# Kernel optimization log

Hardware: AMD Instinct MI355X
Metric: run time of the kernel (lower is better)

Reference implementation:

```python
import jax, jax.numpy as jnp
import numpy as np
from jax.ops import segment_sum, segment_max

# Graph layout: B contiguous graphs of NPER nodes each
N, B, NPER, E, K = 32768, 32, 1024, 524288, 32
IN_DIM, HID = 64, 64
H1, H2 = 4, 2
NEG_ATTN, NEG_ACT = 0.2, 0.01  # DGL GATConv leaky slope; module's LeakyReLU slope


def _gat(x, src, dst, W, al, ar, H, D):
    # DGL GATConv, no bias, no residual, dropout=0
    f = (x @ W).reshape(N, H, D)                      # [N,H,D]
    el = jnp.einsum('nhd,hd->nh', f, al)              # src attention term
    er = jnp.einsum('nhd,hd->nh', f, ar)              # dst attention term
    e = jax.nn.leaky_relu(el[src] + er[dst], NEG_ATTN)  # [E,H]
    m = segment_max(e, dst, num_segments=N)
    m = jnp.where(jnp.isfinite(m), m, 0.0)            # guard isolated nodes
    p = jnp.exp(e - m[dst])
    z = segment_sum(p, dst, num_segments=N)
    a = p / jnp.maximum(z[dst], 1e-9)                 # edge softmax over in-edges
    return segment_sum(a[:, :, None] * f[src], dst, num_segments=N)  # [N,H,D]


def _graphnorm(x, alpha, gamma, beta, eps=1e-5):
    # GraphNorm (Cai et al.): per-graph node normalization with learnable mean scale
    xb = x.reshape(B, NPER, *x.shape[1:])
    mean = xb.mean(axis=1, keepdims=True)
    c = xb - alpha * mean
    var = (c * c).mean(axis=1, keepdims=True)
    return (gamma * c / jnp.sqrt(var + eps) + beta).reshape(x.shape)


def _sortpool(x):
    # DGL SortPooling: sort each node's features ascending, pick top-K nodes by last channel
    xs = jnp.sort(x, axis=-1).reshape(B, NPER, -1)
    _, idx = jax.lax.top_k(xs[:, :, -1], K)           # [B,K]
    sel = jnp.take_along_axis(xs, idx[:, :, None], axis=1)  # [B,K,D]
    return sel.reshape(B, -1)


def setup_inputs() -> dict:
    key = jax.random.key(0)
    ks = jax.random.split(key, 16)
    rng = np.random.default_rng(0)
    # edges constrained within each contiguous graph block
    g = rng.integers(0, B, size=E)
    src = (g * NPER + rng.integers(0, NPER, size=E)).astype(np.int32)
    dst = (g * NPER + rng.integers(0, NPER, size=E)).astype(np.int32)
    s = 0.05
    return {
        'features': jax.random.normal(ks[0], (N, IN_DIM), jnp.float32),
        'src': jnp.asarray(src), 'dst': jnp.asarray(dst),
        'W1': jax.random.normal(ks[1], (IN_DIM, H1 * HID), jnp.float32) * s,
        'al1': jax.random.normal(ks[2], (H1, HID), jnp.float32) * s,
        'ar1': jax.random.normal(ks[3], (H1, HID), jnp.float32) * s,
        'W2': jax.random.normal(ks[4], (H1 * HID, H2 * HID), jnp.float32) * s,
        'al2': jax.random.normal(ks[5], (H2, HID), jnp.float32) * s,
        'ar2': jax.random.normal(ks[6], (H2, HID), jnp.float32) * s,
        'gn1_alpha': jnp.ones((HID,), jnp.float32),
        'gn1_gamma': jnp.ones((HID,), jnp.float32),
        'gn1_beta': jnp.zeros((HID,), jnp.float32),
        'gn2_alpha': jnp.ones((HID,), jnp.float32),
        'gn2_gamma': jnp.ones((HID,), jnp.float32),
        'gn2_beta': jnp.zeros((HID,), jnp.float32),
        'fc1_w': jax.random.normal(ks[7], (2 * K * HID, K * HID), jnp.float32) * 0.02,
        'fc1_b': jnp.zeros((K * HID,), jnp.float32),
        'fc2_w': jax.random.normal(ks[8], (K * HID, 16), jnp.float32) * 0.02,
        'fc2_b': jnp.zeros((16,), jnp.float32),
    }


def reference(features, src, dst, W1, al1, ar1, W2, al2, ar2,
              gn1_alpha, gn1_gamma, gn1_beta, gn2_alpha, gn2_gamma, gn2_beta,
              fc1_w, fc1_b, fc2_w, fc2_b):
    h1 = _gat(features, src, dst, W1, al1, ar1, H1, HID)          # [N,4,HID]
    h1 = jax.nn.leaky_relu(_graphnorm(h1, gn1_alpha, gn1_gamma, gn1_beta), NEG_ACT)
    r1 = _sortpool(h1.mean(1))                                    # [B,K*HID]
    h2 = _gat(h1.reshape(N, -1), src, dst, W2, al2, ar2, H2, HID)  # [N,2,HID]
    h2 = jax.nn.leaky_relu(_graphnorm(h2, gn2_alpha, gn2_gamma, gn2_beta), NEG_ACT)
    r = jnp.concatenate([r1, _sortpool(h2.mean(1))], axis=1)      # [B,2*K*HID]
    hidden = jax.nn.relu(r @ fc1_w + fc1_b)
    return hidden @ fc2_w + fc2_b                                 # [B,16]
```

## Files before the change

kernel.cpp:

```cpp
#include <hip/hip_runtime.h>
#include <math.h>

#define NNODES 32768
#define NGRAPH 32
#define NPERG  1024
#define KSEL   32
#define FC1_KS 64

__device__ inline float wave_reduce_sum(float v) {
  #pragma unroll
  for (int off = 32; off > 0; off >>= 1) v += __shfl_xor(v, off, 64);
  return v;
}
__device__ inline float wave_reduce_max(float v) {
  #pragma unroll
  for (int off = 32; off > 0; off >>= 1) v = fmaxf(v, __shfl_xor(v, off, 64));
  return v;
}

__global__ void csr_count(const int* __restrict__ dst, int* __restrict__ counts, int E_) {
  int e = blockIdx.x * 256 + threadIdx.x;
  if (e < E_) atomicAdd(&counts[dst[e]], 1);
}

__global__ void csr_scan(const int* __restrict__ counts, int* __restrict__ rowptr,
                         int* __restrict__ cursor) {
  __shared__ int partial[256];
  int tid = threadIdx.x;
  int base = tid * 128;
  int s = 0;
  for (int i = 0; i < 128; ++i) s += counts[base + i];
  partial[tid] = s;
  __syncthreads();
  for (int off = 1; off < 256; off <<= 1) {
    int t = (tid >= off) ? partial[tid - off] : 0;
    __syncthreads();
    partial[tid] += t;
    __syncthreads();
  }
  int run = partial[tid] - s;
  for (int i = 0; i < 128; ++i) {
    int c = counts[base + i];
    rowptr[base + i] = run;
    cursor[base + i] = run;
    run += c;
  }
  if (tid == 255) rowptr[NNODES] = run;
}

__global__ void csr_fill(const int* __restrict__ src, const int* __restrict__ dst,
                         int* __restrict__ cursor, int* __restrict__ csrsrc, int E_) {
  int e = blockIdx.x * 256 + threadIdx.x;
  if (e < E_) {
    int p = atomicAdd(&cursor[dst[e]], 1);
    csrsrc[p] = src[e];
  }
}

template <int K, int C, int H>
__global__ __launch_bounds__(256) void gemm_fused(
    const float* __restrict__ X, const float* __restrict__ W,
    const float* __restrict__ al, const float* __restrict__ ar,
    float* __restrict__ F, float* __restrict__ el, float* __restrict__ er) {
  __shared__ float Xs[16][68];
  __shared__ float Ws[16][64];
  __shared__ float redl[64][16];
  __shared__ float redr[64][16];
  const int tid = threadIdx.x;
  const int tx = tid & 15, ty = tid >> 4;
  const int bx = blockIdx.x;
  const int xcd = bx & 7, pos = bx >> 3;
  const int gph = xcd + (pos >> 4) * 8;
  const int row0 = (gph * 16 + (pos & 15)) * 64;
  const int col0 = blockIdx.y * 64;

  float acc[4][4];
  #pragma unroll
  for (int i = 0; i < 4; ++i)
    #pragma unroll
    for (int j = 0; j < 4; ++j) acc[i][j] = 0.f;

  const int rld = tid >> 2;
  const int kq = (tid & 3) * 4;
  const int kw = tid >> 4;
  const int cw = (tid & 15) * 4;

  for (int kt = 0; kt < K; kt += 16) {
    float4 xv = *(const float4*)&X[(size_t)(row0 + rld) * K + kt + kq];
    Xs[kq + 0][rld] = xv.x; Xs[kq + 1][rld] = xv.y;
    Xs[kq + 2][rld] = xv.z; Xs[kq + 3][rld] = xv.w;
    *(float4*)&Ws[kw][cw] = *(const float4*)&W[(size_t)(kt + kw) * C + col0 + cw];
    __syncthreads();
    #pragma unroll
    for (int k = 0; k < 16; ++k) {
      float xr[4], wr[4];
      #pragma unroll
      for (int i = 0; i < 4; ++i) xr[i] = Xs[k][ty * 4 + i];
      #pragma unroll
      for (int j = 0; j < 4; ++j) wr[j] = Ws[k][tx * 4 + j];
      #pragma unroll
      for (int i = 0; i < 4; ++i)
        #pragma unroll
        for (int j = 0; j < 4; ++j) acc[i][j] = fmaf(xr[i], wr[j], acc[i][j]);
    }
    __syncthreads();
  }

  float av[4], rv[4];
  #pragma unroll
  for (int j = 0; j < 4; ++j) { av[j] = al[col0 + tx * 4 + j]; rv[j] = ar[col0 + tx * 4 + j]; }
  #pragma unroll
  for (int i = 0; i < 4; ++i) {
    float4 o = make_float4(acc[i][0], acc[i][1], acc[i][2], acc[i][3]);
    *(float4*)&F[(size_t)(row0 + ty * 4 + i) * C + col0 + tx * 4] = o;
    float pl = acc[i][0] * av[0] + acc[i][1] * av[1] + acc[i][2] * av[2] + acc[i][3] * av[3];
    float pr = acc[i][0] * rv[0] + acc[i][1] * rv[1] + acc[i][2] * rv[2] + acc[i][3] * rv[3];
    redl[ty * 4 + i][tx] = pl;
    redr[ty * 4 + i][tx] = pr;
  }
  __syncthreads();
  if (tid < 64) {
    float s = 0.f, t = 0.f;
    #pragma unroll
    for (int x = 0; x < 16; ++x) { s += redl[tid][x]; t += redr[tid][x]; }
    el[(row0 + tid) * H + blockIdx.y] = s;
    er[(row0 + tid) * H + blockIdx.y] = t;
  }
}

template <int H>
__device__ inline void load_ev(const float* __restrict__ el, int s, float* ev) {
  if constexpr (H == 4) {
    float4 t = *(const float4*)(el + (size_t)s * 4);
    ev[0] = t.x; ev[1] = t.y; ev[2] = t.z; ev[3] = t.w;
  } else {
    float2 t = *(const float2*)(el + (size_t)s * 2);
    ev[0] = t.x; ev[1] = t.y;
  }
}

template <int H>
__global__ __launch_bounds__(256) void gat_agg(
    const float* __restrict__ F, const float* __restrict__ el,
    const float* __restrict__ er, const int* __restrict__ rowptr,
    const int* __restrict__ csrsrc, float* __restrict__ out) {
  __shared__ float plds[4][64][H];
  __shared__ int slds[4][64];
  const int wave = threadIdx.x >> 6;
  const int lane = threadIdx.x & 63;
  const int wg = blockIdx.x;
  const int xcd = wg & 7, pos = wg >> 3;
  const int g = xcd + (pos >> 8) * 8;
  const int n = g * NPERG + (pos & 255) * 4 + wave;
  const int beg = rowptr[n], end = rowptr[n + 1];
  const int hsel = (H == 4) ? (lane >> 4) : (lane >> 5);

  float erh[H];
  #pragma unroll
  for (int h = 0; h < H; ++h) erh[h] = er[n * H + h];

  float e0[H], mx[H];
  #pragma unroll
  for (int h = 0; h < H; ++h) e0[h] = -INFINITY;
  const int i0 = beg + lane;
  int s0 = 0;
  if (i0 < end) {
    s0 = csrsrc[i0];
    float ev[H];
    load_ev<H>(el, s0, ev);
    #pragma unroll
    for (int h = 0; h < H; ++h) {
      float e = ev[h] + erh[h];
      e0[h] = e >= 0.f ? e : 0.2f * e;
    }
  }
  #pragma unroll
  for (int h = 0; h < H; ++h) mx[h] = e0[h];
  for (int i = i0 + 64; i < end; i += 64) {
    int s = csrsrc[i];
    float ev[H];
    load_ev<H>(el, s, ev);
    #pragma unroll
    for (int h = 0; h < H; ++h) {
      float e = ev[h] + erh[h];
      e = e >= 0.f ? e : 0.2f * e;
      mx[h] = fmaxf(mx[h], e);
    }
  }
  #pragma unroll
  for (int h = 0; h < H; ++h) mx[h] = wave_reduce_max(mx[h]);

  float accv[H];
  float psum[H];
  #pragma unroll
  for (int h = 0; h < H; ++h) { accv[h] = 0.f; psum[h] = 0.f; }

  for (int cbeg = beg; cbeg < end; cbeg += 64) {
    int cnt = end - cbeg;
    if (cnt > 64) cnt = 64;
    float pv[H];
    int s = 0;
    #pragma unroll
    for (int h = 0; h < H; ++h) pv[h] = 0.f;
    if (lane < cnt) {
      if (cbeg == beg) {
        s = s0;
        #pragma unroll
        for (int h = 0; h < H; ++h) pv[h] = __expf(e0[h] - mx[h]);
      } else {
        s = csrsrc[cbeg + lane];
        float ev[H];
        load_ev<H>(el, s, ev);
        #pragma unroll
        for (int h = 0; h < H; ++h) {
          float e = ev[h] + erh[h];
          e = e >= 0.f ? e : 0.2f * e;
          pv[h] = __expf(e - mx[h]);
        }
      }
    }
    #pragma unroll
    for (int h = 0; h < H; ++h) psum[h] += wave_reduce_sum(pv[h]);
    slds[wave][lane] = s;
    if constexpr (H == 4)
      *(float4*)&plds[wave][lane][0] = make_float4(pv[0], pv[1], pv[2], pv[3]);
    else
      *(float2*)&plds[wave][lane][0] = make_float2(pv[0], pv[1]);
    __builtin_amdgcn_s_waitcnt(0);

    int j = 0;
    for (; j + 4 <= cnt; j += 4) {
      int ss0 = slds[wave][j + 0], ss1 = slds[wave][j + 1];
      int ss2 = slds[wave][j + 2], ss3 = slds[wave][j + 3];
      float pb0 = plds[wave][j + 0][hsel], pb1 = plds[wave][j + 1][hsel];
      float pb2 = plds[wave][j + 2][hsel], pb3 = plds[wave][j + 3][hsel];
      if constexpr (H == 4) {
        float4 f0 = *(const float4*)&F[(size_t)ss0 * 256 + lane * 4];
        float4 f1 = *(const float4*)&F[(size_t)ss1 * 256 + lane * 4];
        float4 f2 = *(const float4*)&F[(size_t)ss2 * 256 + lane * 4];
        float4 f3 = *(const float4*)&F[(size_t)ss3 * 256 + lane * 4];
        accv[0] = fmaf(pb0, f0.x, accv[0]); accv[1] = fmaf(pb0, f0.y, accv[1]);
        accv[2] = fmaf(pb0, f0.z, accv[2]); accv[3] = fmaf(pb0, f0.w, accv[3]);
        accv[0] = fmaf(pb1, f1.x, accv[0]); accv[1] = fmaf(pb1, f1.y, accv[1]);
        accv[2] = fmaf(pb1, f1.z, accv[2]); accv[3] = fmaf(pb1, f1.w, accv[3]);
        accv[0] = fmaf(pb2, f2.x, accv[0]); accv[1] = fmaf(pb2, f2.y, accv[1]);
        accv[2] = fmaf(pb2, f2.z, accv[2]); accv[3] = fmaf(pb2, f2.w, accv[3]);
        accv[0] = fmaf(pb3, f3.x, accv[0]); accv[1] = fmaf(pb3, f3.y, accv[1]);
        accv[2] = fmaf(pb3, f3.z, accv[2]); accv[3] = fmaf(pb3, f3.w, accv[3]);
      } else {
        float2 f0 = *(const float2*)&F[(size_t)ss0 * 128 + lane * 2];
        float2 f1 = *(const float2*)&F[(size_t)ss1 * 128 + lane * 2];
        float2 f2 = *(const float2*)&F[(size_t)ss2 * 128 + lane * 2];
        float2 f3 = *(const float2*)&F[(size_t)ss3 * 128 + lane * 2];
        accv[0] = fmaf(pb0, f0.x, accv[0]); accv[1] = fmaf(pb0, f0.y, accv[1]);
        accv[0] = fmaf(pb1, f1.x, accv[0]); accv[1] = fmaf(pb1, f1.y, accv[1]);
        accv[0] = fmaf(pb2, f2.x, accv[0]); accv[1] = fmaf(pb2, f2.y, accv[1]);
        accv[0] = fmaf(pb3, f3.x, accv[0]); accv[1] = fmaf(pb3, f3.y, accv[1]);
      }
    }
    for (; j < cnt; ++j) {
      int ss = slds[wave][j];
      float pb = plds[wave][j][hsel];
      if constexpr (H == 4) {
        float4 fv = *(const float4*)&F[(size_t)ss * 256 + lane * 4];
        accv[0] = fmaf(pb, fv.x, accv[0]); accv[1] = fmaf(pb, fv.y, accv[1]);
        accv[2] = fmaf(pb, fv.z, accv[2]); accv[3] = fmaf(pb, fv.w, accv[3]);
      } else {
        float2 fv = *(const float2*)&F[(size_t)ss * 128 + lane * 2];
        accv[0] = fmaf(pb, fv.x, accv[0]); accv[1] = fmaf(pb, fv.y, accv[1]);
      }
    }
  }

  float z;
  if constexpr (H == 4)
    z = hsel == 0 ? psum[0] : hsel == 1 ? psum[1] : hsel == 2 ? psum[2] : psum[3];
  else
    z = hsel == 0 ? psum[0] : psum[1];
  float inv = 1.0f / fmaxf(z, 1e-9f);
  if constexpr (H == 4) {
    float4 o = make_float4(accv[0] * inv, accv[1] * inv, accv[2] * inv, accv[3] * inv);
    *(float4*)&out[(size_t)n * 256 + lane * 4] = o;
  } else {
    float2 o = make_float2(accv[0] * inv, accv[1] * inv);
    *(float2*)&out[(size_t)n * 128 + lane * 2] = o;
  }
}

template <int C>
__global__ void gn_stats_partial(const float* __restrict__ X, float* __restrict__ ps,
                                 float* __restrict__ ps2) {
  const int id = blockIdx.x;
  const int xcd = id & 7, pos = id >> 3;
  const int b = xcd + (pos >> 4) * 8;
  const int sgm = pos & 15;
  int ch = threadIdx.x;
  const float* p = X + ((size_t)b * NPERG + sgm * 64) * C + ch;
  float sx = 0.f, sx2 = 0.f;
  for (int i = 0; i < 64; ++i) { float x = p[(size_t)i * C]; sx += x; sx2 += x * x; }
  ps[(b * 16 + sgm) * C + ch] = sx;
  ps2[(b * 16 + sgm) * C + ch] = sx2;
}

template <int C>
__global__ void gn_stats_final(const float* __restrict__ ps, const float* __restrict__ ps2,
                               const float* __restrict__ alpha, const float* __restrict__ gamma,
                               const float* __restrict__ beta, float* __restrict__ scale,
                               float* __restrict__ shift) {
  int b = blockIdx.x, ch = threadIdx.x;
  float sx = 0.f, sx2 = 0.f;
  for (int s = 0; s < 16; ++s) { sx += ps[(b * 16 + s) * C + ch]; sx2 += ps2[(b * 16 + s) * C + ch]; }
  const float inv = 1.0f / (float)NPERG;
  float mu = sx * inv;
  int d = ch & 63;
  float a = alpha[d];
  float var = sx2 * inv - mu * mu * a * (2.f - a);
  float sc = gamma[d] / sqrtf(var + 1e-5f);
  scale[b * C + ch] = sc;
  shift[b * C + ch] = beta[d] - sc * a * mu;
}

__global__ void gn_apply1(const float* __restrict__ h1, const float* __restrict__ scale,
                          const float* __restrict__ shift, float* __restrict__ h1n,
                          float* __restrict__ meanv, float* __restrict__ keyb) {
  const int wg = blockIdx.x;
  const int xcd = wg & 7, pos = wg >> 3;
  const int g = xcd + (pos >> 8) * 8;
  const int n = g * NPERG + (pos & 255) * 4 + (threadIdx.x >> 6);
  const int d = threadIdx.x & 63;
  const int b = g;
  float s = 0.f;
  #pragma unroll
  for (int h = 0; h < 4; ++h) {
    int ch = h * 64 + d;
    float y = scale[b * 256 + ch] * h1[(size_t)n * 256 + ch] + shift[b * 256 + ch];
    y = y >= 0.f ? y : 0.01f * y;
    h1n[(size_t)n * 256 + ch] = y;
    s += y;
  }
  float m = 0.25f * s;
  meanv[(size_t)n * 64 + d] = m;
  float key = wave_reduce_max(m);
  if (d == 0) keyb[n] = key;
}

__global__ void gn_apply2(const float* __restrict__ h2, const float* __restrict__ scale,
                          const float* __restrict__ shift, float* __restrict__ meanv,
                          float* __restrict__ keyb) {
  const int wg = blockIdx.x;
  const int xcd = wg & 7, pos = wg >> 3;
  const int g = xcd + (pos >> 8) * 8;
  const int n = g * NPERG + (pos & 255) * 4 + (threadIdx.x >> 6);
  const int d = threadIdx.x & 63;
  const int b = g;
  float s = 0.f;
  #pragma unroll
  for (int h = 0; h < 2; ++h) {
    int ch = h * 64 + d;
    float y = scale[b * 128 + ch] * h2[(size_t)n * 128 + ch] + shift[b * 128 + ch];
    y = y >= 0.f ? y : 0.01f * y;
    s += y;
  }
  float m = 0.5f * s;
  meanv[(size_t)n * 64 + d] = m;
  float key = wave_reduce_max(m);
  if (d == 0) keyb[n] = key;
}

__global__ __launch_bounds__(1024) void topk_sort(const float* __restrict__ keyb,
                                                  int* __restrict__ topk) {
  __shared__ unsigned long long lds[NPERG];
  const int b = blockIdx.x, tid = threadIdx.x;
  float f = keyb[b * NPERG + tid];
  unsigned int u = __float_as_uint(f);
  u = (u & 0x80000000u) ? ~u : (u | 0x80000000u);
  unsigned long long v = ((unsigned long long)u << 32) | (unsigned int)(NPERG - 1 - tid);
  for (int kk = 2; kk <= NPERG; kk <<= 1) {
    for (int j = kk >> 1; j > 0; j >>= 1) {
      unsigned long long o;
      if (j >= 64) {
        lds[tid] = v;
        __syncthreads();
        o = lds[tid ^ j];
        __syncthreads();
      } else {
        o = __shfl_xor(v, j, 64);
      }
      bool lower = (tid & j) == 0;
      bool desc = (tid & kk) == 0;
      unsigned long long mx = v > o ? v : o;
      unsigned long long mn = v > o ? o : v;
      v = (lower == desc) ? mx : mn;
    }
  }
  if (tid < KSEL) topk[b * KSEL + tid] = (int)(NPERG - 1 - (unsigned int)(v & 0xFFFFFFFFu));
}

__global__ void sortsel(const float* __restrict__ meanv, const int* __restrict__ topk,
                        float* __restrict__ r, int roff) {
  int wid = (blockIdx.x * blockDim.x + threadIdx.x) >> 6;
  int lane = threadIdx.x & 63;
  int b = wid >> 5, k = wid & 31;
  int node = topk[b * KSEL + k];
  float v = meanv[((size_t)(b * NPERG + node)) * 64 + lane];
  #pragma unroll
  for (int kk = 2; kk <= 64; kk <<= 1) {
    #pragma unroll
    for (int j = kk >> 1; j > 0; j >>= 1) {
      float o = __shfl_xor(v, j, 64);
      bool lower = (lane & j) == 0;
      bool asc = (lane & kk) == 0;
      v = (lower == asc) ? fminf(v, o) : fmaxf(v, o);
    }
  }
  r[(size_t)b * 4096 + roff + k * 64 + lane] = v;
}

__global__ __launch_bounds__(256) void fc1_partial(const float* __restrict__ r,
                                                   const float* __restrict__ w,
                                                   float* __restrict__ part) {
  __shared__ float rs_t[64][36];
  const int ks = blockIdx.x, nb = blockIdx.y;
  const int tid = threadIdx.x;
  const int tx = tid & 63;
  const int ty = tid >> 6;

  #pragma unroll
  for (int t = 0; t < 8; ++t) {
    int elem = t * 256 + tid;
    int m = elem >> 6, k = elem & 63;
    rs_t[k][m] = r[(size_t)m * 4096 + ks * 64 + k];
  }
  __syncthreads();

  const float* wp = w + (size_t)(ks * 64) * 2048 + nb * 256 + tx * 4;
  float4 acc[8];
  #pragma unroll
  for (int i = 0; i < 8; ++i) acc[i] = make_float4(0.f, 0.f, 0.f, 0.f);

  #pragma unroll 4
  for (int k = 0; k < 64; ++k) {
    float4 wv = *(const float4*)&wp[(size_t)k * 2048];
    float4 ra = *(const float4*)&rs_t[k][ty * 8];
    float4 rb = *(const float4*)&rs_t[k][ty * 8 + 4];
    float rr[8] = {ra.x, ra.y, ra.z, ra.w, rb.x, rb.y, rb.z, rb.w};
    #pragma unroll
    for (int i = 0; i < 8; ++i) {
      acc[i].x = fmaf(rr[i], wv.x, acc[i].x);
      acc[i].y = fmaf(rr[i], wv.y, acc[i].y);
      acc[i].z = fmaf(rr[i], wv.z, acc[i].z);
      acc[i].w = fmaf(rr[i], wv.w, acc[i].w);
    }
  }

  #pragma unroll
  for (int i = 0; i < 8; ++i) {
    int m = ty * 8 + i;
    *(float4*)&part[((size_t)ks * 32 + m) * 2048 + nb * 256 + tx * 4] = acc[i];
  }
}

__global__ __launch_bounds__(256) void fc1_reduce(const float* __restrict__ part,
                                                  const float* __restrict__ bias,
                                                  float* __restrict__ hidden) {
  int idx = blockIdx.x * 256 + threadIdx.x;
  int m = idx >> 9, n4 = idx & 511;
  const float* pp = part + (size_t)m * 2048 + n4 * 4;
  float4 b4 = *(const float4*)&bias[n4 * 4];
  float4 s = b4;
  #pragma unroll 8
  for (int ks = 0; ks < FC1_KS; ++ks) {
    float4 v = *(const float4*)&pp[(size_t)ks * 32 * 2048];
    s.x += v.x; s.y += v.y; s.z += v.z; s.w += v.w;
  }
  s.x = fmaxf(s.x, 0.f); s.y = fmaxf(s.y, 0.f);
  s.z = fmaxf(s.z, 0.f); s.w = fmaxf(s.w, 0.f);
  *(float4*)&hidden[(size_t)m * 2048 + n4 * 4] = s;
}

__global__ void fc2_kernel(const float* __restrict__ hidden, const float* __restrict__ w,
                           const float* __restrict__ bias, float* __restrict__ out) {
  int wid = (blockIdx.x * blockDim.x + threadIdx.x) >> 6;
  int lane = threadIdx.x & 63;
  int m = wid >> 4, o = wid & 15;
  float s = 0.f;
  for (int k = lane; k < 2048; k += 64) s = fmaf(hidden[(size_t)m * 2048 + k], w[k * 16 + o], s);
  s = wave_reduce_sum(s);
  if (lane == 0) out[m * 16 + o] = s + bias[o];
}

extern "C" void kernel_launch(void* const* d_in, const int* in_sizes, int n_in,
                              void* d_out, int out_size, void* d_ws, size_t ws_size,
                              hipStream_t stream) {
  const float* features = (const float*)d_in[0];
  const int* src = (const int*)d_in[1];
  const int* dst = (const int*)d_in[2];
  const float* W1 = (const float*)d_in[3];
  const float* al1 = (const float*)d_in[4];
  const float* ar1 = (const float*)d_in[5];
  const float* W2 = (const float*)d_in[6];
  const float* al2 = (const float*)d_in[7];
  const float* ar2 = (const float*)d_in[8];
  const float* gn1a = (const float*)d_in[9];
  const float* gn1g = (const float*)d_in[10];
  const float* gn1b = (const float*)d_in[11];
  const float* gn2a = (const float*)d_in[12];
  const float* gn2g = (const float*)d_in[13];
  const float* gn2b = (const float*)d_in[14];
  const float* fc1w = (const float*)d_in[15];
  const float* fc1b = (const float*)d_in[16];
  const float* fc2w = (const float*)d_in[17];
  const float* fc2b = (const float*)d_in[18];
  float* out = (float*)d_out;
  const int E_ = in_sizes[1];

  float* ws = (float*)d_ws;
  size_t off = 0;
  float* A = ws + off;      off += (size_t)NNODES * 256;
  float* Bb = ws + off;     off += (size_t)NNODES * 256;
  float* meanv = ws + off;  off += (size_t)NNODES * 64;
  float* el1 = ws + off;    off += (size_t)NNODES * 4;
  float* er1 = ws + off;    off += (size_t)NNODES * 4;
  float* el2 = ws + off;    off += (size_t)NNODES * 2;
  float* er2 = ws + off;    off += (size_t)NNODES * 2;
  float* sc1 = ws + off;    off += 32 * 256;
  float* sh1 = ws + off;    off += 32 * 256;
  float* sc2 = ws + off;    off += 32 * 128;
  float* sh2 = ws + off;    off += 32 * 128;
  float* ps = ws + off;     off += 32 * 16 * 256;
  float* ps2 = ws + off;    off += 32 * 16 * 256;
  float* rbuf = ws + off;   off += 32 * 4096;
  float* keyb = ws + off;   off += NNODES;
  int* ibase = (int*)(ws + off);
  int* counts = ibase;
  int* rowptr = counts + NNODES;
  int* cursor = rowptr + NNODES + 1;
  int* csrsrc = cursor + NNODES;
  int* tk1 = csrsrc + E_;
  int* tk2 = tk1 + NGRAPH * KSEL;

  float* f1 = A;
  float* h1n = A;
  float* h1 = Bb;
  float* f2 = Bb;
  float* h2 = Bb + (size_t)NNODES * 128;
  float* part = A;
  float* hidden = A + (size_t)FC1_KS * 32 * 2048;

  hipMemsetAsync(counts, 0, NNODES * sizeof(int), stream);
  csr_count<<<(E_ + 255) / 256, 256, 0, stream>>>(dst, counts, E_);
  csr_scan<<<1, 256, 0, stream>>>(counts, rowptr, cursor);
  csr_fill<<<(E_ + 255) / 256, 256, 0, stream>>>(src, dst, cursor, csrsrc, E_);

  dim3 g1(NNODES / 64, 4);
  gemm_fused<64, 256, 4><<<g1, 256, 0, stream>>>(features, W1, al1, ar1, f1, el1, er1);
  gat_agg<4><<<NNODES / 4, 256, 0, stream>>>(f1, el1, er1, rowptr, csrsrc, h1);

  gn_stats_partial<256><<<NGRAPH * 16, 256, 0, stream>>>(h1, ps, ps2);
  gn_stats_final<256><<<NGRAPH, 256, 0, stream>>>(ps, ps2, gn1a, gn1g, gn1b, sc1, sh1);
  gn_apply1<<<NNODES / 4, 256, 0, stream>>>(h1, sc1, sh1, h1n, meanv, keyb);

  topk_sort<<<NGRAPH, 1024, 0, stream>>>(keyb, tk1);
  sortsel<<<256, 256, 0, stream>>>(meanv, tk1, rbuf, 0);

  dim3 g2(NNODES / 64, 2);
  gemm_fused<256, 128, 2><<<g2, 256, 0, stream>>>(h1n, W2, al2, ar2, f2, el2, er2);
  gat_agg<2><<<NNODES / 4, 256, 0, stream>>>(f2, el2, er2, rowptr, csrsrc, h2);

  gn_stats_partial<128><<<NGRAPH * 16, 128, 0, stream>>>(h2, ps, ps2);
  gn_stats_final<128><<<NGRAPH, 128, 0, stream>>>(ps, ps2, gn2a, gn2g, gn2b, sc2, sh2);
  gn_apply2<<<NNODES / 4, 256, 0, stream>>>(h2, sc2, sh2, meanv, keyb);

  topk_sort<<<NGRAPH, 1024, 0, stream>>>(keyb, tk2);
  sortsel<<<256, 256, 0, stream>>>(meanv, tk2, rbuf, 2048);

  dim3 gfc(FC1_KS, 8);
  fc1_partial<<<gfc, 256, 0, stream>>>(rbuf, fc1w, part);
  fc1_reduce<<<32 * 2048 / 1024, 256, 0, stream>>>(part, fc1b, hidden);
  fc2_kernel<<<128, 256, 0, stream>>>(hidden, fc2w, fc2b, out);
}
```

Before: 274.6 us.

## Drop meanv buffer, recompute mean in sortsel, and deepen gat_agg gather unroll

The gn_apply kernels no longer write a per-node mean vector. The sortsel kernels now recompute the head-mean only for the selected top-K nodes, reading h1n or re-applying the GraphNorm scale and shift to h2. This removes a full N×64 write and its read-back. In gat_agg, source indices and probabilities are packed into one interleaved LDS array and the gather loop unrolls to 8 neighbours, aiming to raise memory-level parallelism at the cost of more registers.

```diff
diff --git a/kernel.cpp b/kernel.cpp
--- a/kernel.cpp
+++ b/kernel.cpp
@@ -144,8 +144,7 @@
     const float* __restrict__ F, const float* __restrict__ el,
     const float* __restrict__ er, const int* __restrict__ rowptr,
     const int* __restrict__ csrsrc, float* __restrict__ out) {
-  __shared__ float plds[4][64][H];
-  __shared__ int slds[4][64];
+  __shared__ float2 eb[4][64][H];
   const int wave = threadIdx.x >> 6;
   const int lane = threadIdx.x & 63;
   const int wg = blockIdx.x;
@@ -190,8 +189,7 @@
   #pragma unroll
   for (int h = 0; h < H; ++h) mx[h] = wave_reduce_max(mx[h]);
 
-  float accv[H];
-  float psum[H];
+  float accv[H], psum[H];
   #pragma unroll
   for (int h = 0; h < H; ++h) { accv[h] = 0.f; psum[h] = 0.f; }
 
@@ -221,52 +219,57 @@
     }
     #pragma unroll
     for (int h = 0; h < H; ++h) psum[h] += wave_reduce_sum(pv[h]);
-    slds[wave][lane] = s;
-    if constexpr (H == 4)
-      *(float4*)&plds[wave][lane][0] = make_float4(pv[0], pv[1], pv[2], pv[3]);
-    else
-      *(float2*)&plds[wave][lane][0] = make_float2(pv[0], pv[1]);
-    __builtin_amdgcn_s_waitcnt(0);
+    float sb = __int_as_float(s);
+    if constexpr (H == 4) {
+      *(float4*)&eb[wave][lane][0] = make_float4(sb, pv[0], sb, pv[1]);
+      *(float4*)&eb[wave][lane][2] = make_float4(sb, pv[2], sb, pv[3]);
+    } else {
+      *(float4*)&eb[wave][lane][0] = make_float4(sb, pv[0], sb, pv[1]);
+    }
+    asm volatile("s_waitcnt lgkmcnt(0)" ::: "memory");
 
     int j = 0;
-    for (; j + 4 <= cnt; j += 4) {
-      int ss0 = slds[wave][j + 0], ss1 = slds[wave][j + 1];
-      int ss2 = slds[wave][j + 2], ss3 = slds[wave][j + 3];
-      float pb0 = plds[wave][j + 0][hsel], pb1 = plds[wave][j + 1][hsel];
-      float pb2 = plds[wave][j + 2][hsel], pb3 = plds[wave][j + 3][hsel];
+    for (; j + 8 <= cnt; j += 8) {
+      float pb[8];
       if constexpr (H == 4) {
-        float4 f0 = *(const float4*)&F[(size_t)ss0 * 256 + lane * 4];
-        float4 f1 = *(const float4*)&F[(size_t)ss1 * 256 + lane * 4];
-        float4 f2 = *(const float4*)&F[(size_t)ss2 * 256 + lane * 4];
-        float4 f3 = *(const float4*)&F[(size_t)ss3 * 256 + lane * 4];
-        accv[0] = fmaf(pb0, f0.x, accv[0]); accv[1] = fmaf(pb0, f0.y, accv[1]);
-        accv[2] = fmaf(pb0, f0.z, accv[2]); accv[3] = fmaf(pb0, f0.w, accv[3]);
-        accv[0] = fmaf(pb1, f1.x, accv[0]); accv[1] = fmaf(pb1, f1.y, accv[1]);
-        accv[2] = fmaf(pb1, f1.z, accv[2]); accv[3] = fmaf(pb1, f1.w, accv[3]);
-        accv[0] = fmaf(pb2, f2.x, accv[0]); accv[1] = fmaf(pb2, f2.y, accv[1]);
-        accv[2] = fmaf(pb2, f2.z, accv[2]); accv[3] = fmaf(pb2, f2.w, accv[3]);
-        accv[0] = fmaf(pb3, f3.x, accv[0]); accv[1] = fmaf(pb3, f3.y, accv[1]);
-        accv[2] = fmaf(pb3, f3.z, accv[2]); accv[3] = fmaf(pb3, f3.w, accv[3]);
+        float4 fv[8];
+        #pragma unroll
+        for (int t = 0; t < 8; ++t) {
+          float2 e = eb[wave][j + t][hsel];
+          pb[t] = e.y;
+          fv[t] = *(const float4*)&F[(size_t)__float_as_int(e.x) * 256 + lane * 4];
+        }
+        #pragma unroll
+        for (int t = 0; t < 8; ++t) {
+          accv[0] = fmaf(pb[t], fv[t].x, accv[0]);
+          accv[1] = fmaf(pb[t], fv[t].y, accv[1]);
+          accv[2] = fmaf(pb[t], fv[t].z, accv[2]);
+          accv[3] = fmaf(pb[t], fv[t].w, accv[3]);
+        }
       } else {
-        float2 f0 = *(const float2*)&F[(size_t)ss0 * 128 + lane * 2];
-        float2 f1 = *(const float2*)&F[(size_t)ss1 * 128 + lane * 2];
-        float2 f2 = *(const float2*)&F[(size_t)ss2 * 128 + lane * 2];
-        float2 f3 = *(const float2*)&F[(size_t)ss3 * 128 + lane * 2];
-        accv[0] = fmaf(pb0, f0.x, accv[0]); accv[1] = fmaf(pb0, f0.y, accv[1]);
-        accv[0] = fmaf(pb1, f1.x, accv[0]); accv[1] = fmaf(pb1, f1.y, accv[1]);
-        accv[0] = fmaf(pb2, f2.x, accv[0]); accv[1] = fmaf(pb2, f2.y, accv[1]);
-        accv[0] = fmaf(pb3, f3.x, accv[0]); accv[1] = fmaf(pb3, f3.y, accv[1]);
+        float2 fv[8];
+        #pragma unroll
+        for (int t = 0; t < 8; ++t) {
+          float2 e = eb[wave][j + t][hsel];
+          pb[t] = e.y;
+          fv[t] = *(const float2*)&F[(size_t)__float_as_int(e.x) * 128 + lane * 2];
+        }
+        #pragma unroll
+        for (int t = 0; t < 8; ++t) {
+          accv[0] = fmaf(pb[t], fv[t].x, accv[0]);
+          accv[1] = fmaf(pb[t], fv[t].y, accv[1]);
+        }
       }
     }
     for (; j < cnt; ++j) {
-      int ss = slds[wave][j];
-      float pb = plds[wave][j][hsel];
+      float2 e = eb[wave][j][hsel];
+      float pb = e.y;
       if constexpr (H == 4) {
-        float4 fv = *(const float4*)&F[(size_t)ss * 256 + lane * 4];
+        float4 fv = *(const float4*)&F[(size_t)__float_as_int(e.x) * 256 + lane * 4];
         accv[0] = fmaf(pb, fv.x, accv[0]); accv[1] = fmaf(pb, fv.y, accv[1]);
         accv[2] = fmaf(pb, fv.z, accv[2]); accv[3] = fmaf(pb, fv.w, accv[3]);
       } else {
-        float2 fv = *(const float2*)&F[(size_t)ss * 128 + lane * 2];
+        float2 fv = *(const float2*)&F[(size_t)__float_as_int(e.x) * 128 + lane * 2];
         accv[0] = fmaf(pb, fv.x, accv[0]); accv[1] = fmaf(pb, fv.y, accv[1]);
       }
     }
@@ -322,30 +325,6 @@
 
 __global__ void gn_apply1(const float* __restrict__ h1, const float* __restrict__ scale,
                           const float* __restrict__ shift, float* __restrict__ h1n,
-                          float* __restrict__ meanv, float* __restrict__ keyb) {
-  const int wg = blockIdx.x;
-  const int xcd = wg & 7, pos = wg >> 3;
-  const int g = xcd + (pos >> 8) * 8;
-  const int n = g * NPERG + (pos & 255) * 4 + (threadIdx.x >> 6);
-  const int d = threadIdx.x & 63;
-  const int b = g;
-  float s = 0.f;
-  #pragma unroll
-  for (int h = 0; h < 4; ++h) {
-    int ch = h * 64 + d;
-    float y = scale[b * 256 + ch] * h1[(size_t)n * 256 + ch] + shift[b * 256 + ch];
-    y = y >= 0.f ? y : 0.01f * y;
-    h1n[(size_t)n * 256 + ch] = y;
-    s += y;
-  }
-  float m = 0.25f * s;
-  meanv[(size_t)n * 64 + d] = m;
-  float key = wave_reduce_max(m);
-  if (d == 0) keyb[n] = key;
-}
-
-__global__ void gn_apply2(const float* __restrict__ h2, const float* __restrict__ scale,
-                          const float* __restrict__ shift, float* __restrict__ meanv,
                           float* __restrict__ keyb) {
   const int wg = blockIdx.x;
   const int xcd = wg & 7, pos = wg >> 3;
@@ -355,15 +334,34 @@
   const int b = g;
   float s = 0.f;
   #pragma unroll
+  for (int h = 0; h < 4; ++h) {
+    int ch = h * 64 + d;
+    float y = scale[b * 256 + ch] * h1[(size_t)n * 256 + ch] + shift[b * 256 + ch];
+    y = y >= 0.f ? y : 0.01f * y;
+    h1n[(size_t)n * 256 + ch] = y;
+    s += y;
+  }
+  float key = wave_reduce_max(0.25f * s);
+  if (d == 0) keyb[n] = key;
+}
+
+__global__ void gn_apply2(const float* __restrict__ h2, const float* __restrict__ scale,
+                          const float* __restrict__ shift, float* __restrict__ keyb) {
+  const int wg = blockIdx.x;
+  const int xcd = wg & 7, pos = wg >> 3;
+  const int g = xcd + (pos >> 8) * 8;
+  const int n = g * NPERG + (pos & 255) * 4 + (threadIdx.x >> 6);
+  const int d = threadIdx.x & 63;
+  const int b = g;
+  float s = 0.f;
+  #pragma unroll
   for (int h = 0; h < 2; ++h) {
     int ch = h * 64 + d;
     float y = scale[b * 128 + ch] * h2[(size_t)n * 128 + ch] + shift[b * 128 + ch];
     y = y >= 0.f ? y : 0.01f * y;
     s += y;
   }
-  float m = 0.5f * s;
-  meanv[(size_t)n * 64 + d] = m;
-  float key = wave_reduce_max(m);
+  float key = wave_reduce_max(0.5f * s);
   if (d == 0) keyb[n] = key;
 }
 
@@ -396,13 +394,7 @@
   if (tid < KSEL) topk[b * KSEL + tid] = (int)(NPERG - 1 - (unsigned int)(v & 0xFFFFFFFFu));
 }
 
-__global__ void sortsel(const float* __restrict__ meanv, const int* __restrict__ topk,
-                        float* __restrict__ r, int roff) {
-  int wid = (blockIdx.x * blockDim.x + threadIdx.x) >> 6;
-  int lane = threadIdx.x & 63;
-  int b = wid >> 5, k = wid & 31;
-  int node = topk[b * KSEL + k];
-  float v = meanv[((size_t)(b * NPERG + node)) * 64 + lane];
+__device__ inline float bitonic_sort64(float v, int lane) {
   #pragma unroll
   for (int kk = 2; kk <= 64; kk <<= 1) {
     #pragma unroll
@@ -413,7 +405,39 @@
       v = (lower == asc) ? fminf(v, o) : fmaxf(v, o);
     }
   }
-  r[(size_t)b * 4096 + roff + k * 64 + lane] = v;
+  return v;
+}
+
+__global__ void sortsel1(const float* __restrict__ h1n, const int* __restrict__ topk,
+                         float* __restrict__ r) {
+  int wid = (blockIdx.x * blockDim.x + threadIdx.x) >> 6;
+  int lane = threadIdx.x & 63;
+  int b = wid >> 5, k = wid & 31;
+  int node = b * NPERG + topk[b * KSEL + k];
+  float s = 0.f;
+  #pragma unroll
+  for (int h = 0; h < 4; ++h) s += h1n[(size_t)node * 256 + h * 64 + lane];
+  float v = bitonic_sort64(0.25f * s, lane);
+  r[(size_t)b * 4096 + k * 64 + lane] = v;
+}
+
+__global__ void sortsel2(const float* __restrict__ h2, const float* __restrict__ scale,
+                         const float* __restrict__ shift, const int* __restrict__ topk,
+                         float* __restrict__ r) {
+  int wid = (blockIdx.x * blockDim.x + threadIdx.x) >> 6;
+  int lane = threadIdx.x & 63;
+  int b = wid >> 5, k = wid & 31;
+  int node = b * NPERG + topk[b * KSEL + k];
+  float s = 0.f;
+  #pragma unroll
+  for (int h = 0; h < 2; ++h) {
+    int ch = h * 64 + lane;
+    float y = scale[b * 128 + ch] * h2[(size_t)node * 128 + ch] + shift[b * 128 + ch];
+    y = y >= 0.f ? y : 0.01f * y;
+    s += y;
+  }
+  float v = bitonic_sort64(0.5f * s, lane);
+  r[(size_t)b * 4096 + 2048 + k * 64 + lane] = v;
 }
 
 __global__ __launch_bounds__(256) void fc1_partial(const float* __restrict__ r,
@@ -518,7 +542,6 @@
   size_t off = 0;
   float* A = ws + off;      off += (size_t)NNODES * 256;
   float* Bb = ws + off;     off += (size_t)NNODES * 256;
-  float* meanv = ws + off;  off += (size_t)NNODES * 64;
   float* el1 = ws + off;    off += (size_t)NNODES * 4;
   float* er1 = ws + off;    off += (size_t)NNODES * 4;
   float* el2 = ws + off;    off += (size_t)NNODES * 2;
@@ -558,10 +581,10 @@
 
   gn_stats_partial<256><<<NGRAPH * 16, 256, 0, stream>>>(h1, ps, ps2);
   gn_stats_final<256><<<NGRAPH, 256, 0, stream>>>(ps, ps2, gn1a, gn1g, gn1b, sc1, sh1);
-  gn_apply1<<<NNODES / 4, 256, 0, stream>>>(h1, sc1, sh1, h1n, meanv, keyb);
+  gn_apply1<<<NNODES / 4, 256, 0, stream>>>(h1, sc1, sh1, h1n, keyb);
 
   topk_sort<<<NGRAPH, 1024, 0, stream>>>(keyb, tk1);
-  sortsel<<<256, 256, 0, stream>>>(meanv, tk1, rbuf, 0);
+  sortsel1<<<256, 256, 0, stream>>>(h1n, tk1, rbuf);
 
   dim3 g2(NNODES / 64, 2);
   gemm_fused<256, 128, 2><<<g2, 256, 0, stream>>>(h1n, W2, al2, ar2, f2, el2, er2);
@@ -569,10 +592,10 @@
 
   gn_stats_partial<128><<<NGRAPH * 16, 128, 0, stream>>>(h2, ps, ps2);
   gn_stats_final<128><<<NGRAPH, 128, 0, stream>>>(ps, ps2, gn2a, gn2g, gn2b, sc2, sh2);
-  gn_apply2<<<NNODES / 4, 256, 0, stream>>>(h2, sc2, sh2, meanv, keyb);
+  gn_apply2<<<NNODES / 4, 256, 0, stream>>>(h2, sc2, sh2, keyb);
 
   topk_sort<<<NGRAPH, 1024, 0, stream>>>(keyb, tk2);
-  sortsel<<<256, 256, 0, stream>>>(meanv, tk2, rbuf, 2048);
+  sortsel2<<<256, 256, 0, stream>>>(h2, sc2, sh2, tk2, rbuf);
 
   dim3 gfc(FC1_KS, 8);
   fc1_partial<<<gfc, 256, 0, stream>>>(rbuf, fc1w, part);
```

New measurement: 285.2 us. +3.9%, slower.

## Drop softmax max pass and recompute node means only for selected top-K nodes

Applied to the files above, without the earlier changes.

The GAT aggregation kernel no longer runs a separate pass over in-edges to find the per-head maximum logit. It exponentiates the leaky-ReLU logits directly, which removes one gather of el per edge and a wave max-reduction. The GraphNorm apply kernels stop writing the full per-node mean array and only emit sort keys. New sortsel kernels recompute the head-mean, and for layer 2 also the normalization, only for the 32 selected nodes per graph. The trade-off is that without max subtraction, exp can overflow if the attention logits grow large, so numerical safety now depends on the logit magnitude.

```diff
diff --git a/kernel.cpp b/kernel.cpp
--- a/kernel.cpp
+++ b/kernel.cpp
@@ -159,39 +159,7 @@
   #pragma unroll
   for (int h = 0; h < H; ++h) erh[h] = er[n * H + h];
 
-  float e0[H], mx[H];
-  #pragma unroll
-  for (int h = 0; h < H; ++h) e0[h] = -INFINITY;
-  const int i0 = beg + lane;
-  int s0 = 0;
-  if (i0 < end) {
-    s0 = csrsrc[i0];
-    float ev[H];
-    load_ev<H>(el, s0, ev);
-    #pragma unroll
-    for (int h = 0; h < H; ++h) {
-      float e = ev[h] + erh[h];
-      e0[h] = e >= 0.f ? e : 0.2f * e;
-    }
-  }
-  #pragma unroll
-  for (int h = 0; h < H; ++h) mx[h] = e0[h];
-  for (int i = i0 + 64; i < end; i += 64) {
-    int s = csrsrc[i];
-    float ev[H];
-    load_ev<H>(el, s, ev);
-    #pragma unroll
-    for (int h = 0; h < H; ++h) {
-      float e = ev[h] + erh[h];
-      e = e >= 0.f ? e : 0.2f * e;
-      mx[h] = fmaxf(mx[h], e);
-    }
-  }
-  #pragma unroll
-  for (int h = 0; h < H; ++h) mx[h] = wave_reduce_max(mx[h]);
-
-  float accv[H];
-  float psum[H];
+  float accv[H], psum[H];
   #pragma unroll
   for (int h = 0; h < H; ++h) { accv[h] = 0.f; psum[h] = 0.f; }
 
@@ -203,20 +171,14 @@
     #pragma unroll
     for (int h = 0; h < H; ++h) pv[h] = 0.f;
     if (lane < cnt) {
-      if (cbeg == beg) {
-        s = s0;
-        #pragma unroll
-        for (int h = 0; h < H; ++h) pv[h] = __expf(e0[h] - mx[h]);
-      } else {
-        s = csrsrc[cbeg + lane];
-        float ev[H];
-        load_ev<H>(el, s, ev);
-        #pragma unroll
-        for (int h = 0; h < H; ++h) {
-          float e = ev[h] + erh[h];
-          e = e >= 0.f ? e : 0.2f * e;
-          pv[h] = __expf(e - mx[h]);
-        }
+      s = csrsrc[cbeg + lane];
+      float ev[H];
+      load_ev<H>(el, s, ev);
+      #pragma unroll
+      for (int h = 0; h < H; ++h) {
+        float e = ev[h] + erh[h];
+        e = e >= 0.f ? e : 0.2f * e;
+        pv[h] = __expf(e);
       }
     }
     #pragma unroll
@@ -322,30 +284,6 @@
 
 __global__ void gn_apply1(const float* __restrict__ h1, const float* __restrict__ scale,
                           const float* __restrict__ shift, float* __restrict__ h1n,
-                          float* __restrict__ meanv, float* __restrict__ keyb) {
-  const int wg = blockIdx.x;
-  const int xcd = wg & 7, pos = wg >> 3;
-  const int g = xcd + (pos >> 8) * 8;
-  const int n = g * NPERG + (pos & 255) * 4 + (threadIdx.x >> 6);
-  const int d = threadIdx.x & 63;
-  const int b = g;
-  float s = 0.f;
-  #pragma unroll
-  for (int h = 0; h < 4; ++h) {
-    int ch = h * 64 + d;
-    float y = scale[b * 256 + ch] * h1[(size_t)n * 256 + ch] + shift[b * 256 + ch];
-    y = y >= 0.f ? y : 0.01f * y;
-    h1n[(size_t)n * 256 + ch] = y;
-    s += y;
-  }
-  float m = 0.25f * s;
-  meanv[(size_t)n * 64 + d] = m;
-  float key = wave_reduce_max(m);
-  if (d == 0) keyb[n] = key;
-}
-
-__global__ void gn_apply2(const float* __restrict__ h2, const float* __restrict__ scale,
-                          const float* __restrict__ shift, float* __restrict__ meanv,
                           float* __restrict__ keyb) {
   const int wg = blockIdx.x;
   const int xcd = wg & 7, pos = wg >> 3;
@@ -355,15 +293,34 @@
   const int b = g;
   float s = 0.f;
   #pragma unroll
+  for (int h = 0; h < 4; ++h) {
+    int ch = h * 64 + d;
+    float y = scale[b * 256 + ch] * h1[(size_t)n * 256 + ch] + shift[b * 256 + ch];
+    y = y >= 0.f ? y : 0.01f * y;
+    h1n[(size_t)n * 256 + ch] = y;
+    s += y;
+  }
+  float key = wave_reduce_max(0.25f * s);
+  if (d == 0) keyb[n] = key;
+}
+
+__global__ void gn_apply2(const float* __restrict__ h2, const float* __restrict__ scale,
+                          const float* __restrict__ shift, float* __restrict__ keyb) {
+  const int wg = blockIdx.x;
+  const int xcd = wg & 7, pos = wg >> 3;
+  const int g = xcd + (pos >> 8) * 8;
+  const int n = g * NPERG + (pos & 255) * 4 + (threadIdx.x >> 6);
+  const int d = threadIdx.x & 63;
+  const int b = g;
+  float s = 0.f;
+  #pragma unroll
   for (int h = 0; h < 2; ++h) {
     int ch = h * 64 + d;
     float y = scale[b * 128 + ch] * h2[(size_t)n * 128 + ch] + shift[b * 128 + ch];
     y = y >= 0.f ? y : 0.01f * y;
     s += y;
   }
-  float m = 0.5f * s;
-  meanv[(size_t)n * 64 + d] = m;
-  float key = wave_reduce_max(m);
+  float key = wave_reduce_max(0.5f * s);
   if (d == 0) keyb[n] = key;
 }
 
@@ -396,13 +353,7 @@
   if (tid < KSEL) topk[b * KSEL + tid] = (int)(NPERG - 1 - (unsigned int)(v & 0xFFFFFFFFu));
 }
 
-__global__ void sortsel(const float* __restrict__ meanv, const int* __restrict__ topk,
-                        float* __restrict__ r, int roff) {
-  int wid = (blockIdx.x * blockDim.x + threadIdx.x) >> 6;
-  int lane = threadIdx.x & 63;
-  int b = wid >> 5, k = wid & 31;
-  int node = topk[b * KSEL + k];
-  float v = meanv[((size_t)(b * NPERG + node)) * 64 + lane];
+__device__ inline float bitonic_sort64(float v, int lane) {
   #pragma unroll
   for (int kk = 2; kk <= 64; kk <<= 1) {
     #pragma unroll
@@ -413,7 +364,39 @@
       v = (lower == asc) ? fminf(v, o) : fmaxf(v, o);
     }
   }
-  r[(size_t)b * 4096 + roff + k * 64 + lane] = v;
+  return v;
+}
+
+__global__ void sortsel1(const float* __restrict__ h1n, const int* __restrict__ topk,
+                         float* __restrict__ r) {
+  int wid = (blockIdx.x * blockDim.x + threadIdx.x) >> 6;
+  int lane = threadIdx.x & 63;
+  int b = wid >> 5, k = wid & 31;
+  int node = b * NPERG + topk[b * KSEL + k];
+  float s = 0.f;
+  #pragma unroll
+  for (int h = 0; h < 4; ++h) s += h1n[(size_t)node * 256 + h * 64 + lane];
+  float v = bitonic_sort64(0.25f * s, lane);
+  r[(size_t)b * 4096 + k * 64 + lane] = v;
+}
+
+__global__ void sortsel2(const float* __restrict__ h2, const float* __restrict__ scale,
+                         const float* __restrict__ shift, const int* __restrict__ topk,
+                         float* __restrict__ r) {
+  int wid = (blockIdx.x * blockDim.x + threadIdx.x) >> 6;
+  int lane = threadIdx.x & 63;
+  int b = wid >> 5, k = wid & 31;
+  int node = b * NPERG + topk[b * KSEL + k];
+  float s = 0.f;
+  #pragma unroll
+  for (int h = 0; h < 2; ++h) {
+    int ch = h * 64 + lane;
+    float y = scale[b * 128 + ch] * h2[(size_t)node * 128 + ch] + shift[b * 128 + ch];
+    y = y >= 0.f ? y : 0.01f * y;
+    s += y;
+  }
+  float v = bitonic_sort64(0.5f * s, lane);
+  r[(size_t)b * 4096 + 2048 + k * 64 + lane] = v;
 }
 
 __global__ __launch_bounds__(256) void fc1_partial(const float* __restrict__ r,
@@ -518,7 +501,6 @@
   size_t off = 0;
   float* A = ws + off;      off += (size_t)NNODES * 256;
   float* Bb = ws + off;     off += (size_t)NNODES * 256;
-  float* meanv = ws + off;  off += (size_t)NNODES * 64;
   float* el1 = ws + off;    off += (size_t)NNODES * 4;
   float* er1 = ws + off;    off += (size_t)NNODES * 4;
   float* el2 = ws + off;    off += (size_t)NNODES * 2;
@@ -558,10 +540,10 @@
 
   gn_stats_partial<256><<<NGRAPH * 16, 256, 0, stream>>>(h1, ps, ps2);
   gn_stats_final<256><<<NGRAPH, 256, 0, stream>>>(ps, ps2, gn1a, gn1g, gn1b, sc1, sh1);
-  gn_apply1<<<NNODES / 4, 256, 0, stream>>>(h1, sc1, sh1, h1n, meanv, keyb);
+  gn_apply1<<<NNODES / 4, 256, 0, stream>>>(h1, sc1, sh1, h1n, keyb);
 
   topk_sort<<<NGRAPH, 1024, 0, stream>>>(keyb, tk1);
-  sortsel<<<256, 256, 0, stream>>>(meanv, tk1, rbuf, 0);
+  sortsel1<<<256, 256, 0, stream>>>(h1n, tk1, rbuf);
 
   dim3 g2(NNODES / 64, 2);
   gemm_fused<256, 128, 2><<<g2, 256, 0, stream>>>(h1n, W2, al2, ar2, f2, el2, er2);
@@ -569,10 +551,10 @@
 
   gn_stats_partial<128><<<NGRAPH * 16, 128, 0, stream>>>(h2, ps, ps2);
   gn_stats_final<128><<<NGRAPH, 128, 0, stream>>>(ps, ps2, gn2a, gn2g, gn2b, sc2, sh2);
-  gn_apply2<<<NNODES / 4, 256, 0, stream>>>(h2, sc2, sh2, meanv, keyb);
+  gn_apply2<<<NNODES / 4, 256, 0, stream>>>(h2, sc2, sh2, keyb);
 
   topk_sort<<<NGRAPH, 1024, 0, stream>>>(keyb, tk2);
-  sortsel<<<256, 256, 0, stream>>>(meanv, tk2, rbuf, 2048);
+  sortsel2<<<256, 256, 0, stream>>>(h2, sc2, sh2, tk2, rbuf);
 
   dim3 gfc(FC1_KS, 8);
   fc1_partial<<<gfc, 256, 0, stream>>>(rbuf, fc1w, part);
```

New measurement: 266.0 us. -3.1%, faster.
